# Kernel tuning notes

Measured on AMD Instinct MI355X. Metric: run time of the kernel, lower is better.

The kernel has to match this reference:

```python
import jax, jax.numpy as jnp
import numpy as np

HIDDEN = 256
HEADS = 8
HEAD_DIM = HIDDEN // HEADS
N = 4096
EPS = 1e-5


def setup_inputs() -> dict:
    key = jax.random.key(0)
    ks = jax.random.split(key, 16)
    s = HIDDEN ** -0.5
    inp = {
        "A": jax.random.uniform(ks[0], (N, N), dtype=jnp.float32),
        "h": jax.random.normal(ks[1], (N, HIDDEN), dtype=jnp.float32),
        # Linear layers stored torch-style as [out, in]
        "Wq": jax.random.normal(ks[2], (HIDDEN, HIDDEN), jnp.float32) * s,
        "bq": jnp.zeros((HIDDEN,), jnp.float32),
        "Wk": jax.random.normal(ks[3], (HIDDEN, HIDDEN), jnp.float32) * s,
        "bk": jnp.zeros((HIDDEN,), jnp.float32),
        "Wv": jax.random.normal(ks[4], (HIDDEN, HIDDEN), jnp.float32) * s,
        "bv": jnp.zeros((HIDDEN,), jnp.float32),
        "Wo": jax.random.normal(ks[5], (HIDDEN, HIDDEN), jnp.float32) * s,
        "bo": jnp.zeros((HIDDEN,), jnp.float32),
        "W1": jax.random.normal(ks[6], (2 * HIDDEN, HIDDEN), jnp.float32) * s,
        "c1": jnp.zeros((2 * HIDDEN,), jnp.float32),
        "W2": jax.random.normal(ks[7], (HIDDEN, 2 * HIDDEN), jnp.float32) * (2 * HIDDEN) ** -0.5,
        "c2": jnp.zeros((HIDDEN,), jnp.float32),
        "g1": jnp.ones((HIDDEN,), jnp.float32),
        "be1": jnp.zeros((HIDDEN,), jnp.float32),
        "g2": jnp.ones((HIDDEN,), jnp.float32),
        "be2": jnp.zeros((HIDDEN,), jnp.float32),
    }
    return inp


def _batchnorm(x, gamma, beta):
    # BatchNorm1d training mode: biased batch stats over node axis
    mean = x.mean(axis=0)
    var = ((x - mean) ** 2).mean(axis=0)
    return (x - mean) * jax.lax.rsqrt(var + EPS) * gamma + beta


def _mha(A, h, Wq, bq, Wk, bk, Wv, bv, Wo, bo):
    n = h.shape[0]
    scaling = HEAD_DIM ** -0.5
    # NOTE: raw reshape [N, H*d] -> (H, N, d), exactly as the torch code (no transpose)
    q = ((h @ Wq.T + bq).reshape(HEADS, n, HEAD_DIM)) * scaling
    k = (h @ Wk.T + bk).reshape(HEADS, n, HEAD_DIM)
    v = (h @ Wv.T + bv).reshape(HEADS, n, HEAD_DIM)
    t = jnp.einsum('hnd,hmd->hnm', q, k)          # [H, N, N]
    attn = jax.nn.softmax(t * A, axis=2)          # multiplicative adjacency mask
    out = jnp.einsum('hnm,hmd->hnd', attn, v)     # [H, N, d]
    return out.reshape(n, -1) @ Wo.T + bo         # raw reshape back, as in torch


def reference(A, h, Wq, bq, Wk, bk, Wv, bv, Wo, bo, W1, c1, W2, c2, g1, be1, g2, be2):
    h1 = h
    x = _mha(A, h, Wq, bq, Wk, bk, Wv, bv, Wo, bo)
    x = _batchnorm(x + h1, g1, be1)
    h2 = x
    x = jax.nn.relu(x @ W1.T + c1) @ W2.T + c2
    return _batchnorm(h2 + x, g2, be2)
```

## Files before the change

### kernel.cpp

```cpp
#include <hip/hip_runtime.h>

#define N_NODES 4096
#define HID 256
#define NHEADS 8
#define HDIM 32
#define EPSV 1e-5f
#define M2LOG 11.541560327111707f

typedef __bf16 bf16x8 __attribute__((ext_vector_type(8)));
typedef __bf16 bf16x4 __attribute__((ext_vector_type(4)));
typedef float f32x4 __attribute__((ext_vector_type(4)));

__device__ inline float fexp2(float x) {
    float r;
    asm("v_exp_f32 %0, %1" : "=v"(r) : "v"(x));
    return r;
}

__device__ inline uint4 pack8(float4 a, float4 b) {
    bf16x8 p;
    p[0]=(__bf16)a.x; p[1]=(__bf16)a.y; p[2]=(__bf16)a.z; p[3]=(__bf16)a.w;
    p[4]=(__bf16)b.x; p[5]=(__bf16)b.y; p[6]=(__bf16)b.z; p[7]=(__bf16)b.w;
    return __builtin_bit_cast(uint4, p);
}
__device__ inline float4 nmad4(float4 x, float4 s, float4 sh) {
    return make_float4(fmaf(x.x,s.x,sh.x), fmaf(x.y,s.y,sh.y),
                       fmaf(x.z,s.z,sh.z), fmaf(x.w,s.w,sh.w));
}

__launch_bounds__(256)
__global__ void gemm_mfma(const float* __restrict__ X, const float* __restrict__ W,
                          const float* __restrict__ bias, const float* __restrict__ resid,
                          float* __restrict__ C,
                          const float* __restrict__ nscale, const float* __restrict__ nshift,
                          const float* __restrict__ rscale, const float* __restrict__ rshift,
                          int M, int N, int K, float scale, int do_relu) {
    __shared__ uint4 xl[2][512];
    __shared__ uint4 wl[2][512];
    const int bm = blockIdx.x * 64, bn = blockIdx.y * 64;
    const int t = threadIdx.x;
    const int w = t >> 6, l = t & 63, g = l >> 4, nl = l & 15;
    const int srow = t >> 3, seg = t & 7;
    const int sx = (seg & 3) << 1;
    const int d0 = seg*64 + (srow ^ sx);
    const int d1 = seg*64 + ((srow + 32) ^ sx);
    const float* xp = X + (size_t)(bm + srow)*K + seg*8;
    const float* wp = W + (size_t)(bn + srow)*K + seg*8;
    const size_t rstep = (size_t)32*K;

    f32x4 acc[4];
    #pragma unroll
    for (int nf = 0; nf < 4; ++nf) acc[nf] = (f32x4){0.f,0.f,0.f,0.f};

    {
        float4 x0 = *(const float4*)(xp),          x1 = *(const float4*)(xp + 4);
        float4 x2 = *(const float4*)(xp + rstep),  x3 = *(const float4*)(xp + rstep + 4);
        if (nscale) {
            float4 s0 = *(const float4*)(nscale + seg*8), s1 = *(const float4*)(nscale + seg*8 + 4);
            float4 h0 = *(const float4*)(nshift + seg*8), h1 = *(const float4*)(nshift + seg*8 + 4);
            x0 = nmad4(x0,s0,h0); x1 = nmad4(x1,s1,h1);
            x2 = nmad4(x2,s0,h0); x3 = nmad4(x3,s1,h1);
        }
        float4 w0 = *(const float4*)(wp),          w1 = *(const float4*)(wp + 4);
        float4 w2 = *(const float4*)(wp + rstep),  w3 = *(const float4*)(wp + rstep + 4);
        xl[0][d0] = pack8(x0, x1); xl[0][d1] = pack8(x2, x3);
        wl[0][d0] = pack8(w0, w1); wl[0][d1] = pack8(w2, w3);
    }
    __syncthreads();

    for (int k0 = 0; k0 < K; k0 += 64) {
        const int cur = (k0 >> 6) & 1;
        const bool nxt = (k0 + 64) < K;
        float4 nx0, nx1, nx2, nx3, nw0, nw1, nw2, nw3;
        if (nxt) {
            const int kk = k0 + 64;
            nx0 = *(const float4*)(xp + kk);          nx1 = *(const float4*)(xp + kk + 4);
            nx2 = *(const float4*)(xp + rstep + kk);  nx3 = *(const float4*)(xp + rstep + kk + 4);
            if (nscale) {
                float4 s0 = *(const float4*)(nscale + kk + seg*8), s1 = *(const float4*)(nscale + kk + seg*8 + 4);
                float4 h0 = *(const float4*)(nshift + kk + seg*8), h1 = *(const float4*)(nshift + kk + seg*8 + 4);
                nx0 = nmad4(nx0,s0,h0); nx1 = nmad4(nx1,s1,h1);
                nx2 = nmad4(nx2,s0,h0); nx3 = nmad4(nx3,s1,h1);
            }
            nw0 = *(const float4*)(wp + kk);          nw1 = *(const float4*)(wp + kk + 4);
            nw2 = *(const float4*)(wp + rstep + kk);  nw3 = *(const float4*)(wp + rstep + kk + 4);
        }
        __builtin_amdgcn_s_setprio(1);
        #pragma unroll
        for (int ks = 0; ks < 2; ++ks) {
            bf16x8 af = __builtin_bit_cast(bf16x8, xl[cur][(ks*4 + g)*64 + ((w*16 + nl) ^ (g << 1))]);
            #pragma unroll
            for (int nf = 0; nf < 4; ++nf) {
                bf16x8 bfr = __builtin_bit_cast(bf16x8, wl[cur][(ks*4 + g)*64 + ((nf*16 + nl) ^ (g << 1))]);
                acc[nf] = __builtin_amdgcn_mfma_f32_16x16x32_bf16(af, bfr, acc[nf], 0, 0, 0);
            }
        }
        __builtin_amdgcn_s_setprio(0);
        if (nxt) {
            xl[cur^1][d0] = pack8(nx0, nx1); xl[cur^1][d1] = pack8(nx2, nx3);
            wl[cur^1][d0] = pack8(nw0, nw1); wl[cur^1][d1] = pack8(nw2, nw3);
        }
        __syncthreads();
    }

    #pragma unroll
    for (int nf = 0; nf < 4; ++nf) {
        const int col = bn + nf*16 + nl;
        const float bb = bias[col];
        float rs = 1.f, rh = 0.f;
        if (rscale) { rs = rscale[col]; rh = rshift[col]; }
        #pragma unroll
        for (int r = 0; r < 4; ++r) {
            const int row = bm + w*16 + g*4 + r;
            float v = acc[nf][r] + bb;
            if (resid) {
                float rv = resid[(size_t)row*N + col];
                v += rscale ? fmaf(rv, rs, rh) : rv;
            }
            v *= scale;
            if (do_relu) v = fmaxf(v, 0.f);
            C[(size_t)row*N + col] = v;
        }
    }
}

__launch_bounds__(256)
__global__ void gemm_qkv(const float* __restrict__ X,
                         const float* __restrict__ Wq, const float* __restrict__ Wk,
                         const float* __restrict__ Wv, const float* __restrict__ bq,
                         const float* __restrict__ bk, const float* __restrict__ bv,
                         __bf16* __restrict__ qhat, __bf16* __restrict__ khat,
                         __bf16* __restrict__ vhat) {
    const int K = 256;
    __shared__ uint4 xl[2][512];
    __shared__ uint4 wl[2][512];
    const int z = blockIdx.z;
    const float* W = (z == 0) ? Wq : (z == 1) ? Wk : Wv;
    const float* bias = (z == 0) ? bq : (z == 1) ? bk : bv;
    __bf16* hat = (z == 0) ? qhat : (z == 1) ? khat : vhat;
    const float scale = (z == 0) ? 0.25506595325f : 1.f;

    const int bm = blockIdx.x * 64, bn = blockIdx.y * 64;
    const int t = threadIdx.x;
    const int w = t >> 6, l = t & 63, g = l >> 4, nl = l & 15;
    const int srow = t >> 3, seg = t & 7;
    const int sx = (seg & 3) << 1;
    const int d0 = seg*64 + (srow ^ sx);
    const int d1 = seg*64 + ((srow + 32) ^ sx);
    const float* xp = X + (size_t)(bm + srow)*K + seg*8;
    const float* wp = W + (size_t)(bn + srow)*K + seg*8;
    const size_t rstep = (size_t)32*K;

    f32x4 acc[4];
    #pragma unroll
    for (int nf = 0; nf < 4; ++nf) acc[nf] = (f32x4){0.f,0.f,0.f,0.f};

    {
        float4 x0 = *(const float4*)(xp),          x1 = *(const float4*)(xp + 4);
        float4 x2 = *(const float4*)(xp + rstep),  x3 = *(const float4*)(xp + rstep + 4);
        float4 w0 = *(const float4*)(wp),          w1 = *(const float4*)(wp + 4);
        float4 w2 = *(const float4*)(wp + rstep),  w3 = *(const float4*)(wp + rstep + 4);
        xl[0][d0] = pack8(x0, x1); xl[0][d1] = pack8(x2, x3);
        wl[0][d0] = pack8(w0, w1); wl[0][d1] = pack8(w2, w3);
    }
    __syncthreads();

    for (int k0 = 0; k0 < K; k0 += 64) {
        const int cur = (k0 >> 6) & 1;
        const bool nxt = (k0 + 64) < K;
        float4 nx0, nx1, nx2, nx3, nw0, nw1, nw2, nw3;
        if (nxt) {
            nx0 = *(const float4*)(xp + k0 + 64);          nx1 = *(const float4*)(xp + k0 + 68);
            nx2 = *(const float4*)(xp + rstep + k0 + 64);  nx3 = *(const float4*)(xp + rstep + k0 + 68);
            nw0 = *(const float4*)(wp + k0 + 64);          nw1 = *(const float4*)(wp + k0 + 68);
            nw2 = *(const float4*)(wp + rstep + k0 + 64);  nw3 = *(const float4*)(wp + rstep + k0 + 68);
        }
        __builtin_amdgcn_s_setprio(1);
        #pragma unroll
        for (int ks = 0; ks < 2; ++ks) {
            bf16x8 af = __builtin_bit_cast(bf16x8, xl[cur][(ks*4 + g)*64 + ((w*16 + nl) ^ (g << 1))]);
            #pragma unroll
            for (int nf = 0; nf < 4; ++nf) {
                bf16x8 bfr = __builtin_bit_cast(bf16x8, wl[cur][(ks*4 + g)*64 + ((nf*16 + nl) ^ (g << 1))]);
                acc[nf] = __builtin_amdgcn_mfma_f32_16x16x32_bf16(af, bfr, acc[nf], 0, 0, 0);
            }
        }
        __builtin_amdgcn_s_setprio(0);
        if (nxt) {
            xl[cur^1][d0] = pack8(nx0, nx1); xl[cur^1][d1] = pack8(nx2, nx3);
            wl[cur^1][d0] = pack8(nw0, nw1); wl[cur^1][d1] = pack8(nw2, nw3);
        }
        __syncthreads();
    }

    #pragma unroll
    for (int nf = 0; nf < 4; ++nf) {
        const int col = bn + nf*16 + nl;
        const float bb = bias[col];
        #pragma unroll
        for (int r = 0; r < 4; ++r) {
            const int row = bm + w*16 + g*4 + r;
            float v = (acc[nf][r] + bb) * scale;
            const int hh = row >> 9;
            const int nn = ((row & 511) << 3) | (col >> 5);
            hat[((size_t)(hh*4096 + nn))*32 + (col & 31)] = (__bf16)v;
        }
    }
}

__launch_bounds__(256)
__global__ void transpose_vhat(const __bf16* __restrict__ vhat, __bf16* __restrict__ vT) {
    const int h = blockIdx.y, n0 = blockIdx.x * 64;
    __shared__ __bf16 tile[64][40];
    const int t = threadIdx.x;
    {
        int n = t >> 2, dd0 = (t & 3) * 8;
        *(uint4*)&tile[n][dd0] = *(const uint4*)(vhat + ((size_t)(h*4096 + n0 + n))*32 + dd0);
    }
    __syncthreads();
    {
        int d = t >> 3, ns = (t & 7) * 8;
        uint4 ov;
        __bf16* op = (__bf16*)&ov;
        #pragma unroll
        for (int j = 0; j < 8; ++j) op[j] = tile[ns + j][d];
        *(uint4*)(vT + ((size_t)(h*32 + d))*4096 + n0 + ns) = ov;
    }
}

__launch_bounds__(512, 2)
__global__ void attn_mfma(const __bf16* __restrict__ qh_, const __bf16* __restrict__ kh,
                          const __bf16* __restrict__ vT, const float* __restrict__ A,
                          float* __restrict__ Opart, float* __restrict__ Lpart, int mlen) {
    __shared__ float A_lds[2][64][68];
    __shared__ uint4 p_lds[8][4][64];

    const int t = threadIdx.x;
    const int w = t >> 6, l = t & 63;
    const int g = l >> 4, nl = l & 15;
    const int n0 = blockIdx.x * 64;
    const int z = blockIdx.y;
    const int m_begin = z * mlen;
    const int nsteps = mlen >> 6;

    bf16x8 qf[4];
    #pragma unroll
    for (int nf = 0; nf < 4; ++nf)
        qf[nf] = *(const bf16x8*)(qh_ + ((size_t)(w*4096 + n0 + nf*16 + nl))*32 + g*8);

    f32x4 oacc[4][2];
    #pragma unroll
    for (int nf = 0; nf < 4; ++nf) {
        oacc[nf][0] = (f32x4){0.f,0.f,0.f,0.f};
        oacc[nf][1] = (f32x4){0.f,0.f,0.f,0.f};
    }
    float Li[4] = {0.f, 0.f, 0.f, 0.f};

    const int aq = t >> 3, am = (t & 7) * 8;
    const float* Abase = A + (size_t)(n0 + aq)*N_NODES + m_begin + am;
    const __bf16* kbase = kh + ((size_t)w*4096 + nl)*32 + g*8;
    const __bf16* vbase = vT + ((size_t)w*32 + nl)*4096 + g*8;

    *(float4*)&A_lds[0][aq][am]   = *(const float4*)(Abase);
    *(float4*)&A_lds[0][aq][am+4] = *(const float4*)(Abase + 4);
    __syncthreads();

    for (int s = 0; s < nsteps; ++s) {
        const int cur = s & 1;
        const int m0 = m_begin + s*64;
        const bool nxt = (s + 1) < nsteps;
        float4 a0n, a1n;
        if (nxt) {
            a0n = *(const float4*)(Abase + (s+1)*64);
            a1n = *(const float4*)(Abase + (s+1)*64 + 4);
        }

        #pragma unroll
        for (int half = 0; half < 2; ++half) {
            const int mh = m0 + half*32;
            bf16x8 vf0 = *(const bf16x8*)(vbase + mh);
            bf16x8 vf1 = *(const bf16x8*)(vbase + (size_t)16*4096 + mh);

            #pragma unroll
            for (int tt2 = 0; tt2 < 2; ++tt2) {
                const int tt = half*2 + tt2;
                bf16x8 kf = *(const bf16x8*)(kbase + (size_t)(m0 + tt*16)*32);
                f32x4 st[4];
                __builtin_amdgcn_s_setprio(1);
                #pragma unroll
                for (int nf = 0; nf < 4; ++nf) {
                    f32x4 zz = (f32x4){0.f,0.f,0.f,0.f};
                    st[nf] = __builtin_amdgcn_mfma_f32_16x16x32_bf16(kf, qf[nf], zz, 0, 0, 0);
                }
                __builtin_amdgcn_s_setprio(0);
                #pragma unroll
                for (int nf = 0; nf < 4; ++nf) {
                    const f32x4 a4 = *(const f32x4*)&A_lds[cur][nf*16 + nl][tt*16 + g*4];
                    float p0 = fexp2(fmaf(st[nf][0], a4[0], -M2LOG));
                    float p1 = fexp2(fmaf(st[nf][1], a4[1], -M2LOG));
                    float p2 = fexp2(fmaf(st[nf][2], a4[2], -M2LOG));
                    float p3 = fexp2(fmaf(st[nf][3], a4[3], -M2LOG));
                    Li[nf] += (p0 + p1) + (p2 + p3);
                    bf16x4 pk;
                    pk[0] = (__bf16)p0; pk[1] = (__bf16)p1;
                    pk[2] = (__bf16)p2; pk[3] = (__bf16)p3;
                    const int gm = tt2*2 + (g >> 1);
                    *(bf16x4*)((char*)&p_lds[w][nf][0] + (gm*16 + (nl ^ (gm << 1)))*16 + (g & 1)*8) = pk;
                }
            }
            __builtin_amdgcn_s_setprio(1);
            #pragma unroll
            for (int nf = 0; nf < 4; ++nf) {
                bf16x8 pf = __builtin_bit_cast(bf16x8, p_lds[w][nf][g*16 + (nl ^ (g << 1))]);
                oacc[nf][0] = __builtin_amdgcn_mfma_f32_16x16x32_bf16(vf0, pf, oacc[nf][0], 0, 0, 0);
                oacc[nf][1] = __builtin_amdgcn_mfma_f32_16x16x32_bf16(vf1, pf, oacc[nf][1], 0, 0, 0);
            }
            __builtin_amdgcn_s_setprio(0);
        }

        if (nxt) {
            *(float4*)&A_lds[cur^1][aq][am]   = a0n;
            *(float4*)&A_lds[cur^1][aq][am+4] = a1n;
        }
        __syncthreads();
    }

    #pragma unroll
    for (int nf = 0; nf < 4; ++nf) {
        Li[nf] += __shfl_xor(Li[nf], 16);
        Li[nf] += __shfl_xor(Li[nf], 32);
        const int nq = n0 + nf*16 + nl;
        float* ob = Opart + ((size_t)(z*NHEADS + w)*4096 + nq)*32;
        *(float4*)(ob + 0*16 + g*4) = make_float4(oacc[nf][0][0], oacc[nf][0][1],
                                                  oacc[nf][0][2], oacc[nf][0][3]);
        *(float4*)(ob + 1*16 + g*4) = make_float4(oacc[nf][1][0], oacc[nf][1][1],
                                                  oacc[nf][1][2], oacc[nf][1][3]);
        if (g == 0)
            Lpart[(z*NHEADS + w)*4096 + nq] = Li[nf];
    }
}

__launch_bounds__(256)
__global__ void attn_combine(const float* __restrict__ Opart, const float* __restrict__ Lpart,
                             float* __restrict__ AO, int nsplit) {
    const int idx4 = (blockIdx.x * 256 + threadIdx.x) * 4;
    const int hn = idx4 >> 5;
    float L = 0.f;
    float4 acc = make_float4(0.f, 0.f, 0.f, 0.f);
    for (int zz = 0; zz < nsplit; ++zz) {
        L += Lpart[zz*32768 + hn];
        float4 o = *(const float4*)(Opart + (size_t)zz*1048576 + idx4);
        acc.x += o.x; acc.y += o.y; acc.z += o.z; acc.w += o.w;
    }
    const float inv = 1.f / L;
    *(float4*)(AO + idx4) = make_float4(acc.x*inv, acc.y*inv, acc.z*inv, acc.w*inv);
}

__launch_bounds__(256)
__global__ void colstats_part(const float* __restrict__ X, float* __restrict__ ps,
                              float* __restrict__ pq) {
    const int b = blockIdx.x, t = threadIdx.x;
    float s = 0.f, q = 0.f;
    const float* p = X + (size_t)b*64*HID + t;
    #pragma unroll 8
    for (int r = 0; r < 64; ++r) {
        float v = p[r*HID];
        s += v; q = fmaf(v, v, q);
    }
    ps[b*HID + t] = s;
    pq[b*HID + t] = q;
}

__launch_bounds__(256)
__global__ void colstats_fin(const float* __restrict__ ps, const float* __restrict__ pq,
                             const float* __restrict__ gam, const float* __restrict__ bet,
                             float* __restrict__ scl, float* __restrict__ shf) {
    const int c = threadIdx.x;
    float s = 0.f, q = 0.f;
    #pragma unroll 8
    for (int b = 0; b < 64; ++b) { s += ps[b*HID + c]; q += pq[b*HID + c]; }
    const float m = s * (1.f/4096.f);
    const float rstd = rsqrtf(q*(1.f/4096.f) - m*m + EPSV);
    const float sc = rstd * gam[c];
    scl[c] = sc;
    shf[c] = fmaf(-m, sc, bet[c]);
}

__launch_bounds__(256)
__global__ void bnorm_apply4(const float* __restrict__ X, const float* __restrict__ scl,
                             const float* __restrict__ shf, float* __restrict__ Y) {
    const int base = (blockIdx.x * 256 + threadIdx.x) * 4;
    const int c = base & (HID - 1);
    float4 x = *(const float4*)(X + base);
    float4 o;
    o.x = fmaf(x.x, scl[c+0], shf[c+0]);
    o.y = fmaf(x.y, scl[c+1], shf[c+1]);
    o.z = fmaf(x.z, scl[c+2], shf[c+2]);
    o.w = fmaf(x.w, scl[c+3], shf[c+3]);
    *(float4*)(Y + base) = o;
}

extern "C" void kernel_launch(void* const* d_in, const int* in_sizes, int n_in,
                              void* d_out, int out_size, void* d_ws, size_t ws_size,
                              hipStream_t stream) {
    const float* A  = (const float*)d_in[0];
    const float* h  = (const float*)d_in[1];
    const float* Wq = (const float*)d_in[2];
    const float* bq = (const float*)d_in[3];
    const float* Wk = (const float*)d_in[4];
    const float* bk = (const float*)d_in[5];
    const float* Wv = (const float*)d_in[6];
    const float* bv = (const float*)d_in[7];
    const float* Wo = (const float*)d_in[8];
    const float* bo = (const float*)d_in[9];
    const float* W1 = (const float*)d_in[10];
    const float* c1 = (const float*)d_in[11];
    const float* W2 = (const float*)d_in[12];
    const float* c2 = (const float*)d_in[13];
    const float* g1 = (const float*)d_in[14];
    const float* be1= (const float*)d_in[15];
    const float* g2 = (const float*)d_in[16];
    const float* be2= (const float*)d_in[17];

    char* wsb = (char*)d_ws;
    const size_t MiB = (size_t)1 << 20;
    const int nsplit = (ws_size >= 43*MiB) ? 8 : (ws_size >= 26*MiB) ? 4 : 2;
    const int mlen = N_NODES / nsplit;

    __bf16* qhat = (__bf16*)(wsb + 0*MiB);
    __bf16* khat = (__bf16*)(wsb + 2*MiB);
    __bf16* vhat = (__bf16*)(wsb + 4*MiB);
    __bf16* vT   = (__bf16*)(wsb + 6*MiB);
    float* Opart = (float*)(wsb + 8*MiB);
    float* Lpart = (float*)(wsb + 8*MiB + (size_t)nsplit*4*MiB);
    char* statb  = wsb + 8*MiB + (size_t)nsplit*4*MiB + 1*MiB;
    float* partS = (float*)statb;
    float* partQ = partS + 64*HID;
    float* scale1 = partQ + 64*HID;
    float* shift1 = scale1 + HID;
    float* scale2 = shift1 + HID;
    float* shift2 = scale2 + HID;
    float* AO = (float*)(wsb + 0*MiB);
    float* Y1 = (float*)(wsb + 4*MiB);
    float* F1 = (float*)(wsb + 8*MiB);
    float* Y2 = (float*)(wsb + 0*MiB);

    gemm_qkv<<<dim3(64, 4, 3), 256, 0, stream>>>(h, Wq, Wk, Wv, bq, bk, bv, qhat, khat, vhat);
    transpose_vhat<<<dim3(64, 8), 256, 0, stream>>>(vhat, vT);

    attn_mfma<<<dim3(64, nsplit), 512, 0, stream>>>(qhat, khat, vT, A, Opart, Lpart, mlen);
    attn_combine<<<1024, 256, 0, stream>>>(Opart, Lpart, AO, nsplit);

    gemm_mfma<<<dim3(64, 4), 256, 0, stream>>>(AO, Wo, bo, h, Y1,
                                               nullptr, nullptr, nullptr, nullptr,
                                               4096, 256, 256, 1.f, 0);

    colstats_part<<<64, 256, 0, stream>>>(Y1, partS, partQ);
    colstats_fin<<<1, 256, 0, stream>>>(partS, partQ, g1, be1, scale1, shift1);

    gemm_mfma<<<dim3(64, 8), 256, 0, stream>>>(Y1, W1, c1, nullptr, F1,
                                               scale1, shift1, nullptr, nullptr,
                                               4096, 512, 256, 1.f, 1);
    gemm_mfma<<<dim3(64, 4), 256, 0, stream>>>(F1, W2, c2, Y1, Y2,
                                               nullptr, nullptr, scale1, shift1,
                                               4096, 256, 512, 1.f, 0);

    colstats_part<<<64, 256, 0, stream>>>(Y2, partS, partQ);
    colstats_fin<<<1, 256, 0, stream>>>(partS, partQ, g2, be2, scale2, shift2);
    bnorm_apply4<<<1024, 256, 0, stream>>>(Y2, scale2, shift2, (float*)d_out);
}
```

Baseline: 133.6 us.

## Halve attention query tile to 32 rows and restructure per-fragment P staging

The attention kernel now processes 32 query rows per block instead of 64 and doubles the grid in x. Each warp computes scores for two key tiles per query fragment, applies exp, stages P in a single per-warp LDS slot, and immediately runs the PV MFMAs. This lowers registers and LDS per block and adds parallelism, which may raise occupancy. The cost is that K and V fragments are reloaded for twice as many query tiles, and the reuse of P staging adds serialization through LDS.

```diff
diff --git a/kernel.cpp b/kernel.cpp
--- a/kernel.cpp
+++ b/kernel.cpp
@@ -232,101 +232,99 @@
 __global__ void attn_mfma(const __bf16* __restrict__ qh_, const __bf16* __restrict__ kh,
                           const __bf16* __restrict__ vT, const float* __restrict__ A,
                           float* __restrict__ Opart, float* __restrict__ Lpart, int mlen) {
-    __shared__ float A_lds[2][64][68];
-    __shared__ uint4 p_lds[8][4][64];
+    __shared__ float A_lds[2][32][68];
+    __shared__ uint4 p_lds[8][64];
 
     const int t = threadIdx.x;
     const int w = t >> 6, l = t & 63;
     const int g = l >> 4, nl = l & 15;
-    const int n0 = blockIdx.x * 64;
+    const int n0 = blockIdx.x * 32;
     const int z = blockIdx.y;
     const int m_begin = z * mlen;
     const int nsteps = mlen >> 6;
 
-    bf16x8 qf[4];
-    #pragma unroll
-    for (int nf = 0; nf < 4; ++nf)
+    bf16x8 qf[2];
+    #pragma unroll
+    for (int nf = 0; nf < 2; ++nf)
         qf[nf] = *(const bf16x8*)(qh_ + ((size_t)(w*4096 + n0 + nf*16 + nl))*32 + g*8);
 
-    f32x4 oacc[4][2];
-    #pragma unroll
-    for (int nf = 0; nf < 4; ++nf) {
+    f32x4 oacc[2][2];
+    #pragma unroll
+    for (int nf = 0; nf < 2; ++nf) {
         oacc[nf][0] = (f32x4){0.f,0.f,0.f,0.f};
         oacc[nf][1] = (f32x4){0.f,0.f,0.f,0.f};
     }
-    float Li[4] = {0.f, 0.f, 0.f, 0.f};
-
-    const int aq = t >> 3, am = (t & 7) * 8;
+    float Li[2] = {0.f, 0.f};
+
+    const int aq = t >> 4, am = (t & 15) * 4;
     const float* Abase = A + (size_t)(n0 + aq)*N_NODES + m_begin + am;
     const __bf16* kbase = kh + ((size_t)w*4096 + nl)*32 + g*8;
     const __bf16* vbase = vT + ((size_t)w*32 + nl)*4096 + g*8;
 
-    *(float4*)&A_lds[0][aq][am]   = *(const float4*)(Abase);
-    *(float4*)&A_lds[0][aq][am+4] = *(const float4*)(Abase + 4);
+    *(float4*)&A_lds[0][aq][am] = *(const float4*)(Abase);
     __syncthreads();
 
     for (int s = 0; s < nsteps; ++s) {
         const int cur = s & 1;
         const int m0 = m_begin + s*64;
         const bool nxt = (s + 1) < nsteps;
-        float4 a0n, a1n;
-        if (nxt) {
-            a0n = *(const float4*)(Abase + (s+1)*64);
-            a1n = *(const float4*)(Abase + (s+1)*64 + 4);
-        }
+        float4 an;
+        if (nxt) an = *(const float4*)(Abase + (s+1)*64);
 
         #pragma unroll
         for (int half = 0; half < 2; ++half) {
             const int mh = m0 + half*32;
+            bf16x8 kf0 = *(const bf16x8*)(kbase + (size_t)mh*32);
+            bf16x8 kf1 = *(const bf16x8*)(kbase + (size_t)(mh + 16)*32);
             bf16x8 vf0 = *(const bf16x8*)(vbase + mh);
             bf16x8 vf1 = *(const bf16x8*)(vbase + (size_t)16*4096 + mh);
 
             #pragma unroll
-            for (int tt2 = 0; tt2 < 2; ++tt2) {
-                const int tt = half*2 + tt2;
-                bf16x8 kf = *(const bf16x8*)(kbase + (size_t)(m0 + tt*16)*32);
-                f32x4 st[4];
+            for (int nf = 0; nf < 2; ++nf) {
+                f32x4 zz = (f32x4){0.f,0.f,0.f,0.f};
                 __builtin_amdgcn_s_setprio(1);
-                #pragma unroll
-                for (int nf = 0; nf < 4; ++nf) {
-                    f32x4 zz = (f32x4){0.f,0.f,0.f,0.f};
-                    st[nf] = __builtin_amdgcn_mfma_f32_16x16x32_bf16(kf, qf[nf], zz, 0, 0, 0);
+                f32x4 st0 = __builtin_amdgcn_mfma_f32_16x16x32_bf16(kf0, qf[nf], zz, 0, 0, 0);
+                f32x4 st1 = __builtin_amdgcn_mfma_f32_16x16x32_bf16(kf1, qf[nf], zz, 0, 0, 0);
+                __builtin_amdgcn_s_setprio(0);
+
+                const int tta = half*2, ttb = half*2 + 1;
+                const f32x4 a40 = *(const f32x4*)&A_lds[cur][nf*16 + nl][tta*16 + g*4];
+                const f32x4 a41 = *(const f32x4*)&A_lds[cur][nf*16 + nl][ttb*16 + g*4];
+                float p0 = fexp2(fmaf(st0[0], a40[0], -M2LOG));
+                float p1 = fexp2(fmaf(st0[1], a40[1], -M2LOG));
+                float p2 = fexp2(fmaf(st0[2], a40[2], -M2LOG));
+                float p3 = fexp2(fmaf(st0[3], a40[3], -M2LOG));
+                float p4 = fexp2(fmaf(st1[0], a41[0], -M2LOG));
+                float p5 = fexp2(fmaf(st1[1], a41[1], -M2LOG));
+                float p6 = fexp2(fmaf(st1[2], a41[2], -M2LOG));
+                float p7 = fexp2(fmaf(st1[3], a41[3], -M2LOG));
+                Li[nf] += ((p0 + p1) + (p2 + p3)) + ((p4 + p5) + (p6 + p7));
+
+                bf16x4 pka, pkb;
+                pka[0] = (__bf16)p0; pka[1] = (__bf16)p1; pka[2] = (__bf16)p2; pka[3] = (__bf16)p3;
+                pkb[0] = (__bf16)p4; pkb[1] = (__bf16)p5; pkb[2] = (__bf16)p6; pkb[3] = (__bf16)p7;
+                {
+                    const int gma = 0*2 + (g >> 1);
+                    const int gmb = 1*2 + (g >> 1);
+                    *(bf16x4*)((char*)&p_lds[w][0] + (gma*16 + (nl ^ (gma << 1)))*16 + (g & 1)*8) = pka;
+                    *(bf16x4*)((char*)&p_lds[w][0] + (gmb*16 + (nl ^ (gmb << 1)))*16 + (g & 1)*8) = pkb;
                 }
-                __builtin_amdgcn_s_setprio(0);
-                #pragma unroll
-                for (int nf = 0; nf < 4; ++nf) {
-                    const f32x4 a4 = *(const f32x4*)&A_lds[cur][nf*16 + nl][tt*16 + g*4];
-                    float p0 = fexp2(fmaf(st[nf][0], a4[0], -M2LOG));
-                    float p1 = fexp2(fmaf(st[nf][1], a4[1], -M2LOG));
-                    float p2 = fexp2(fmaf(st[nf][2], a4[2], -M2LOG));
-                    float p3 = fexp2(fmaf(st[nf][3], a4[3], -M2LOG));
-                    Li[nf] += (p0 + p1) + (p2 + p3);
-                    bf16x4 pk;
-                    pk[0] = (__bf16)p0; pk[1] = (__bf16)p1;
-                    pk[2] = (__bf16)p2; pk[3] = (__bf16)p3;
-                    const int gm = tt2*2 + (g >> 1);
-                    *(bf16x4*)((char*)&p_lds[w][nf][0] + (gm*16 + (nl ^ (gm << 1)))*16 + (g & 1)*8) = pk;
-                }
-            }
-            __builtin_amdgcn_s_setprio(1);
-            #pragma unroll
-            for (int nf = 0; nf < 4; ++nf) {
-                bf16x8 pf = __builtin_bit_cast(bf16x8, p_lds[w][nf][g*16 + (nl ^ (g << 1))]);
+                bf16x8 pf = __builtin_bit_cast(bf16x8, p_lds[w][g*16 + (nl ^ (g << 1))]);
+                __builtin_amdgcn_s_setprio(1);
                 oacc[nf][0] = __builtin_amdgcn_mfma_f32_16x16x32_bf16(vf0, pf, oacc[nf][0], 0, 0, 0);
                 oacc[nf][1] = __builtin_amdgcn_mfma_f32_16x16x32_bf16(vf1, pf, oacc[nf][1], 0, 0, 0);
+                __builtin_amdgcn_s_setprio(0);
             }
-            __builtin_amdgcn_s_setprio(0);
         }
 
         if (nxt) {
-            *(float4*)&A_lds[cur^1][aq][am]   = a0n;
-            *(float4*)&A_lds[cur^1][aq][am+4] = a1n;
+            *(float4*)&A_lds[cur^1][aq][am] = an;
         }
         __syncthreads();
     }
 
     #pragma unroll
-    for (int nf = 0; nf < 4; ++nf) {
+    for (int nf = 0; nf < 2; ++nf) {
         Li[nf] += __shfl_xor(Li[nf], 16);
         Li[nf] += __shfl_xor(Li[nf], 32);
         const int nq = n0 + nf*16 + nl;
@@ -448,7 +446,7 @@
     gemm_qkv<<<dim3(64, 4, 3), 256, 0, stream>>>(h, Wq, Wk, Wv, bq, bk, bv, qhat, khat, vhat);
     transpose_vhat<<<dim3(64, 8), 256, 0, stream>>>(vhat, vT);
 
-    attn_mfma<<<dim3(64, nsplit), 512, 0, stream>>>(qhat, khat, vT, A, Opart, Lpart, mlen);
+    attn_mfma<<<dim3(128, nsplit), 512, 0, stream>>>(qhat, khat, vT, A, Opart, Lpart, mlen);
     attn_combine<<<1024, 256, 0, stream>>>(Opart, Lpart, AO, nsplit);
 
     gemm_mfma<<<dim3(64, 4), 256, 0, stream>>>(AO, Wo, bo, h, Y1,
```

Result: slower. 136.6 us (+2.3%).

## Fuse attention combine and column stats into GEMM epilogues, prefetch K/V fragments

Applied to the files above, without the earlier changes.

Adds a gemm_wo kernel that reduces the split-K attention partials (sum of O parts divided by summed L) while loading its A operand, which removes the separate attn_combine kernel and its AO round trip. Batch-norm column partial sums and sums of squares are now computed in the GEMM epilogues through an LDS reduction, which removes two colstats_part launches and their re-reads of Y1 and Y2. The attention loop now loads all K and V fragments for a step up front, behind a sched barrier. In exchange, each Wo GEMM tile re-reads the Opart partials for every column block (four times), and the hoisted fragments raise register pressure.

```diff
diff --git a/kernel.cpp b/kernel.cpp
--- a/kernel.cpp
+++ b/kernel.cpp
@@ -34,6 +34,7 @@
                           float* __restrict__ C,
                           const float* __restrict__ nscale, const float* __restrict__ nshift,
                           const float* __restrict__ rscale, const float* __restrict__ rshift,
+                          float* __restrict__ psum, float* __restrict__ pq,
                           int M, int N, int K, float scale, int do_relu) {
     __shared__ uint4 xl[2][512];
     __shared__ uint4 wl[2][512];
@@ -103,6 +104,7 @@
         __syncthreads();
     }
 
+    float colS[4] = {0.f,0.f,0.f,0.f}, colQ[4] = {0.f,0.f,0.f,0.f};
     #pragma unroll
     for (int nf = 0; nf < 4; ++nf) {
         const int col = bn + nf*16 + nl;
@@ -120,6 +122,140 @@
             v *= scale;
             if (do_relu) v = fmaxf(v, 0.f);
             C[(size_t)row*N + col] = v;
+            colS[nf] += v;
+            colQ[nf] = fmaf(v, v, colQ[nf]);
+        }
+    }
+    if (psum) {
+        float* cs = (float*)&xl[0][0];
+        float* cq = cs + 1024;
+        #pragma unroll
+        for (int nf = 0; nf < 4; ++nf) {
+            const int idx = (w*4 + g)*64 + nf*16 + nl;
+            cs[idx] = colS[nf];
+            cq[idx] = colQ[nf];
+        }
+        __syncthreads();
+        if (t < 64) {
+            float s = 0.f, q = 0.f;
+            #pragma unroll
+            for (int i = 0; i < 16; ++i) { s += cs[i*64 + t]; q += cq[i*64 + t]; }
+            psum[blockIdx.x*HID + bn + t] = s;
+            pq[blockIdx.x*HID + bn + t]   = q;
+        }
+    }
+}
+
+__launch_bounds__(256)
+__global__ void gemm_wo(const float* __restrict__ Opart, const float* __restrict__ Lpart,
+                        int nsplit, const float* __restrict__ W,
+                        const float* __restrict__ bias, const float* __restrict__ resid,
+                        float* __restrict__ C, float* __restrict__ psum, float* __restrict__ pq) {
+    const int N = 256, K = 256;
+    __shared__ uint4 xl[2][512];
+    __shared__ uint4 wl[2][512];
+    const int bm = blockIdx.x * 64, bn = blockIdx.y * 64;
+    const int t = threadIdx.x;
+    const int w = t >> 6, l = t & 63, g = l >> 4, nl = l & 15;
+    const int srow = t >> 3, seg = t & 7;
+    const int sx = (seg & 3) << 1;
+    const int d0 = seg*64 + (srow ^ sx);
+    const int d1 = seg*64 + ((srow + 32) ^ sx);
+    const float* wp = W + (size_t)(bn + srow)*K + seg*8;
+    const size_t rstep = (size_t)32*K;
+
+    auto cl = [&](int row, int kk, float4& a, float4& b) {
+        const size_t flat = (size_t)row*256 + kk;
+        const int hn = (int)(flat >> 5);
+        float L = 0.f;
+        a = make_float4(0.f,0.f,0.f,0.f);
+        b = make_float4(0.f,0.f,0.f,0.f);
+        for (int z = 0; z < nsplit; ++z) {
+            L += Lpart[z*32768 + hn];
+            float4 u = *(const float4*)(Opart + (size_t)z*1048576 + flat);
+            float4 v = *(const float4*)(Opart + (size_t)z*1048576 + flat + 4);
+            a.x += u.x; a.y += u.y; a.z += u.z; a.w += u.w;
+            b.x += v.x; b.y += v.y; b.z += v.z; b.w += v.w;
+        }
+        const float inv = 1.f / L;
+        a.x *= inv; a.y *= inv; a.z *= inv; a.w *= inv;
+        b.x *= inv; b.y *= inv; b.z *= inv; b.w *= inv;
+    };
+
+    f32x4 acc[4];
+    #pragma unroll
+    for (int nf = 0; nf < 4; ++nf) acc[nf] = (f32x4){0.f,0.f,0.f,0.f};
+
+    {
+        float4 x0, x1, x2, x3;
+        cl(bm + srow,      seg*8, x0, x1);
+        cl(bm + srow + 32, seg*8, x2, x3);
+        float4 w0 = *(const float4*)(wp),          w1 = *(const float4*)(wp + 4);
+        float4 w2 = *(const float4*)(wp + rstep),  w3 = *(const float4*)(wp + rstep + 4);
+        xl[0][d0] = pack8(x0, x1); xl[0][d1] = pack8(x2, x3);
+        wl[0][d0] = pack8(w0, w1); wl[0][d1] = pack8(w2, w3);
+    }
+    __syncthreads();
+
+    for (int k0 = 0; k0 < K; k0 += 64) {
+        const int cur = (k0 >> 6) & 1;
+        const bool nxt = (k0 + 64) < K;
+        float4 nx0, nx1, nx2, nx3, nw0, nw1, nw2, nw3;
+        if (nxt) {
+            const int kk = k0 + 64 + seg*8;
+            cl(bm + srow,      kk, nx0, nx1);
+            cl(bm + srow + 32, kk, nx2, nx3);
+            nw0 = *(const float4*)(wp + k0 + 64);          nw1 = *(const float4*)(wp + k0 + 68);
+            nw2 = *(const float4*)(wp + rstep + k0 + 64);  nw3 = *(const float4*)(wp + rstep + k0 + 68);
+        }
+        __builtin_amdgcn_s_setprio(1);
+        #pragma unroll
+        for (int ks = 0; ks < 2; ++ks) {
+            bf16x8 af = __builtin_bit_cast(bf16x8, xl[cur][(ks*4 + g)*64 + ((w*16 + nl) ^ (g << 1))]);
+            #pragma unroll
+            for (int nf = 0; nf < 4; ++nf) {
+                bf16x8 bfr = __builtin_bit_cast(bf16x8, wl[cur][(ks*4 + g)*64 + ((nf*16 + nl) ^ (g << 1))]);
+                acc[nf] = __builtin_amdgcn_mfma_f32_16x16x32_bf16(af, bfr, acc[nf], 0, 0, 0);
+            }
+        }
+        __builtin_amdgcn_s_setprio(0);
+        if (nxt) {
+            xl[cur^1][d0] = pack8(nx0, nx1); xl[cur^1][d1] = pack8(nx2, nx3);
+            wl[cur^1][d0] = pack8(nw0, nw1); wl[cur^1][d1] = pack8(nw2, nw3);
+        }
+        __syncthreads();
+    }
+
+    float colS[4] = {0.f,0.f,0.f,0.f}, colQ[4] = {0.f,0.f,0.f,0.f};
+    #pragma unroll
+    for (int nf = 0; nf < 4; ++nf) {
+        const int col = bn + nf*16 + nl;
+        const float bb = bias[col];
+        #pragma unroll
+        for (int r = 0; r < 4; ++r) {
+            const int row = bm + w*16 + g*4 + r;
+            float v = acc[nf][r] + bb + resid[(size_t)row*N + col];
+            C[(size_t)row*N + col] = v;
+            colS[nf] += v;
+            colQ[nf] = fmaf(v, v, colQ[nf]);
+        }
+    }
+    {
+        float* cs = (float*)&xl[0][0];
+        float* cq = cs + 1024;
+        #pragma unroll
+        for (int nf = 0; nf < 4; ++nf) {
+            const int idx = (w*4 + g)*64 + nf*16 + nl;
+            cs[idx] = colS[nf];
+            cq[idx] = colQ[nf];
+        }
+        __syncthreads();
+        if (t < 64) {
+            float s = 0.f, q = 0.f;
+            #pragma unroll
+            for (int i = 0; i < 16; ++i) { s += cs[i*64 + t]; q += cq[i*64 + t]; }
+            psum[blockIdx.x*HID + bn + t] = s;
+            pq[blockIdx.x*HID + bn + t]   = q;
         }
     }
 }
@@ -274,23 +410,28 @@
             a0n = *(const float4*)(Abase + (s+1)*64);
             a1n = *(const float4*)(Abase + (s+1)*64 + 4);
         }
+        bf16x8 kf[4], vf[4];
+        #pragma unroll
+        for (int tt = 0; tt < 4; ++tt)
+            kf[tt] = *(const bf16x8*)(kbase + (size_t)(m0 + tt*16)*32);
+        #pragma unroll
+        for (int half = 0; half < 2; ++half)
+            #pragma unroll
+            for (int dt = 0; dt < 2; ++dt)
+                vf[half*2+dt] = *(const bf16x8*)(vbase + (size_t)dt*16*4096 + m0 + half*32);
+        __builtin_amdgcn_sched_barrier(0);
 
         #pragma unroll
         for (int half = 0; half < 2; ++half) {
-            const int mh = m0 + half*32;
-            bf16x8 vf0 = *(const bf16x8*)(vbase + mh);
-            bf16x8 vf1 = *(const bf16x8*)(vbase + (size_t)16*4096 + mh);
-
             #pragma unroll
             for (int tt2 = 0; tt2 < 2; ++tt2) {
                 const int tt = half*2 + tt2;
-                bf16x8 kf = *(const bf16x8*)(kbase + (size_t)(m0 + tt*16)*32);
                 f32x4 st[4];
                 __builtin_amdgcn_s_setprio(1);
                 #pragma unroll
                 for (int nf = 0; nf < 4; ++nf) {
                     f32x4 zz = (f32x4){0.f,0.f,0.f,0.f};
-                    st[nf] = __builtin_amdgcn_mfma_f32_16x16x32_bf16(kf, qf[nf], zz, 0, 0, 0);
+                    st[nf] = __builtin_amdgcn_mfma_f32_16x16x32_bf16(kf[tt], qf[nf], zz, 0, 0, 0);
                 }
                 __builtin_amdgcn_s_setprio(0);
                 #pragma unroll
@@ -312,8 +453,8 @@
             #pragma unroll
             for (int nf = 0; nf < 4; ++nf) {
                 bf16x8 pf = __builtin_bit_cast(bf16x8, p_lds[w][nf][g*16 + (nl ^ (g << 1))]);
-                oacc[nf][0] = __builtin_amdgcn_mfma_f32_16x16x32_bf16(vf0, pf, oacc[nf][0], 0, 0, 0);
-                oacc[nf][1] = __builtin_amdgcn_mfma_f32_16x16x32_bf16(vf1, pf, oacc[nf][1], 0, 0, 0);
+                oacc[nf][0] = __builtin_amdgcn_mfma_f32_16x16x32_bf16(vf[half*2+0], pf, oacc[nf][0], 0, 0, 0);
+                oacc[nf][1] = __builtin_amdgcn_mfma_f32_16x16x32_bf16(vf[half*2+1], pf, oacc[nf][1], 0, 0, 0);
             }
             __builtin_amdgcn_s_setprio(0);
         }
@@ -338,37 +479,6 @@
         if (g == 0)
             Lpart[(z*NHEADS + w)*4096 + nq] = Li[nf];
     }
-}
-
-__launch_bounds__(256)
-__global__ void attn_combine(const float* __restrict__ Opart, const float* __restrict__ Lpart,
-                             float* __restrict__ AO, int nsplit) {
-    const int idx4 = (blockIdx.x * 256 + threadIdx.x) * 4;
-    const int hn = idx4 >> 5;
-    float L = 0.f;
-    float4 acc = make_float4(0.f, 0.f, 0.f, 0.f);
-    for (int zz = 0; zz < nsplit; ++zz) {
-        L += Lpart[zz*32768 + hn];
-        float4 o = *(const float4*)(Opart + (size_t)zz*1048576 + idx4);
-        acc.x += o.x; acc.y += o.y; acc.z += o.z; acc.w += o.w;
-    }
-    const float inv = 1.f / L;
-    *(float4*)(AO + idx4) = make_float4(acc.x*inv, acc.y*inv, acc.z*inv, acc.w*inv);
-}
-
-__launch_bounds__(256)
-__global__ void colstats_part(const float* __restrict__ X, float* __restrict__ ps,
-                              float* __restrict__ pq) {
-    const int b = blockIdx.x, t = threadIdx.x;
-    float s = 0.f, q = 0.f;
-    const float* p = X + (size_t)b*64*HID + t;
-    #pragma unroll 8
-    for (int r = 0; r < 64; ++r) {
-        float v = p[r*HID];
-        s += v; q = fmaf(v, v, q);
-    }
-    ps[b*HID + t] = s;
-    pq[b*HID + t] = q;
 }
 
 __launch_bounds__(256)
@@ -440,7 +550,6 @@
     float* shift1 = scale1 + HID;
     float* scale2 = shift1 + HID;
     float* shift2 = scale2 + HID;
-    float* AO = (float*)(wsb + 0*MiB);
     float* Y1 = (float*)(wsb + 4*MiB);
     float* F1 = (float*)(wsb + 8*MiB);
     float* Y2 = (float*)(wsb + 0*MiB);
@@ -449,23 +558,16 @@
     transpose_vhat<<<dim3(64, 8), 256, 0, stream>>>(vhat, vT);
 
     attn_mfma<<<dim3(64, nsplit), 512, 0, stream>>>(qhat, khat, vT, A, Opart, Lpart, mlen);
-    attn_combine<<<1024, 256, 0, stream>>>(Opart, Lpart, AO, nsplit);
-
-    gemm_mfma<<<dim3(64, 4), 256, 0, stream>>>(AO, Wo, bo, h, Y1,
-                                               nullptr, nullptr, nullptr, nullptr,
-                                               4096, 256, 256, 1.f, 0);
-
-    colstats_part<<<64, 256, 0, stream>>>(Y1, partS, partQ);
+
+    gemm_wo<<<dim3(64, 4), 256, 0, stream>>>(Opart, Lpart, nsplit, Wo, bo, h, Y1, partS, partQ);
     colstats_fin<<<1, 256, 0, stream>>>(partS, partQ, g1, be1, scale1, shift1);
 
     gemm_mfma<<<dim3(64, 8), 256, 0, stream>>>(Y1, W1, c1, nullptr, F1,
                                                scale1, shift1, nullptr, nullptr,
-                                               4096, 512, 256, 1.f, 1);
+                                               nullptr, nullptr, 4096, 512, 256, 1.f, 1);
     gemm_mfma<<<dim3(64, 4), 256, 0, stream>>>(F1, W2, c2, Y1, Y2,
                                                nullptr, nullptr, scale1, shift1,
-                                               4096, 256, 512, 1.f, 0);
-
-    colstats_part<<<64, 256, 0, stream>>>(Y2, partS, partQ);
+                                               partS, partQ, 4096, 256, 512, 1.f, 0);
     colstats_fin<<<1, 256, 0, stream>>>(partS, partQ, g2, be2, scale2, shift2);
     bnorm_apply4<<<1024, 256, 0, stream>>>(Y2, scale2, shift2, (float*)d_out);
 }
```

Measured after the change: 130.2 us. 1.03x faster.
